# Optimization experiments

Hardware: AMD Instinct MI355X
Metric: run time of the kernel (lower is better)

Reference implementation:

```python
import jax, jax.numpy as jnp
import numpy as np

DIM = 6
HID = 8
N_UT = DIM * (DIM - 1) // 2  # 15


def setup_inputs() -> dict:
    key = jax.random.key(0)
    ks = jax.random.split(key, 13)
    B, T = 256, 4096
    x = jax.random.normal(ks[0], (B, T, DIM), dtype=jnp.float32)

    def kaiming(k, fan_out, fan_in):
        std = np.sqrt(2.0 / fan_in)
        return jax.random.normal(k, (fan_out, fan_in), dtype=jnp.float32) * std

    inp = {
        "x": x,
        "W_in": kaiming(ks[1], HID, DIM),
        "b_in": jnp.zeros((HID,), jnp.float32),
        "W1": kaiming(ks[2], HID, HID), "b1": jnp.zeros((HID,), jnp.float32),
        "W2": kaiming(ks[3], HID, HID), "b2": jnp.zeros((HID,), jnp.float32),
        "W3": kaiming(ks[4], HID, HID), "b3": jnp.zeros((HID,), jnp.float32),
        "W4": kaiming(ks[5], HID, HID), "b4": jnp.zeros((HID,), jnp.float32),
        "W_out": kaiming(ks[6], N_UT, HID),
        "b_out": jnp.zeros((N_UT,), jnp.float32),
    }
    return inp


def reference(x, W_in, b_in, W1, b1, W2, b2, W3, b3, W4, b4, W_out, b_out):
    B, T, dim = x.shape
    xf = x.reshape(B * T, dim)
    sp = jax.nn.softplus
    y = sp(xf @ W_in.T + b_in)
    y = sp(y @ W1.T + b1)
    y = sp(y @ W2.T + b2)
    y = sp(y @ W3.T + b3)
    y = sp(y @ W4.T + b4)
    ut = y @ W_out.T + b_out  # [N, dim*(dim-1)/2]
    iu, ju = jnp.triu_indices(dim, k=1)  # row-major order matches torch loop
    L = jnp.zeros((B * T, dim, dim), dtype=x.dtype)
    L = L.at[:, iu, ju].set(ut)
    L = L.at[:, ju, iu].set(-ut)
    return L.reshape(B, T, dim, dim)
```

## Files before the change

### kernel.cpp

```cpp
#include <hip/hip_runtime.h>

#define DEV_INLINE __device__ __forceinline__

DEV_INLINE float softplus_f(float v) {
    return fmaxf(v, 0.0f) + __logf(1.0f + __expf(-fabsf(v)));
}

__global__ __launch_bounds__(256) void pb_kernel(
    const float* __restrict__ x,
    const float* __restrict__ W_in, const float* __restrict__ b_in,
    const float* __restrict__ W1,   const float* __restrict__ b1,
    const float* __restrict__ W2,   const float* __restrict__ b2,
    const float* __restrict__ W3,   const float* __restrict__ b3,
    const float* __restrict__ W4,   const float* __restrict__ b4,
    const float* __restrict__ W_out,const float* __restrict__ b_out,
    float* __restrict__ out, int n_pairs)
{
    const int tid = blockIdx.x * blockDim.x + threadIdx.x;
    if (tid >= n_pairs) return;

    const float4* xv = (const float4*)x + (size_t)tid * 3;
    float4 a0 = xv[0];
    float4 a1 = xv[1];
    float4 a2 = xv[2];
    float xin[2][6] = {
        { a0.x, a0.y, a0.z, a0.w, a1.x, a1.y },
        { a1.z, a1.w, a2.x, a2.y, a2.z, a2.w }
    };

    float y[2][8];
    #pragma unroll
    for (int r = 0; r < 2; ++r) {
        #pragma unroll
        for (int o = 0; o < 8; ++o) {
            float acc = b_in[o];
            #pragma unroll
            for (int i = 0; i < 6; ++i)
                acc = fmaf(W_in[o * 6 + i], xin[r][i], acc);
            y[r][o] = softplus_f(acc);
        }
    }

    const float* Ws[4] = { W1, W2, W3, W4 };
    const float* bs[4] = { b1, b2, b3, b4 };
    #pragma unroll
    for (int l = 0; l < 4; ++l) {
        const float* __restrict__ W = Ws[l];
        const float* __restrict__ b = bs[l];
        float t[2][8];
        #pragma unroll
        for (int r = 0; r < 2; ++r) {
            #pragma unroll
            for (int o = 0; o < 8; ++o) {
                float acc = b[o];
                #pragma unroll
                for (int i = 0; i < 8; ++i)
                    acc = fmaf(W[o * 8 + i], y[r][i], acc);
                t[r][o] = softplus_f(acc);
            }
        }
        #pragma unroll
        for (int r = 0; r < 2; ++r)
            #pragma unroll
            for (int o = 0; o < 8; ++o)
                y[r][o] = t[r][o];
    }

    float4* ov = (float4*)out + (size_t)tid * 18;
    #pragma unroll
    for (int r = 0; r < 2; ++r) {
        float u[15];
        #pragma unroll
        for (int o = 0; o < 15; ++o) {
            float acc = b_out[o];
            #pragma unroll
            for (int i = 0; i < 8; ++i)
                acc = fmaf(W_out[o * 8 + i], y[r][i], acc);
            u[o] = acc;
        }

        float L[36];
        #pragma unroll
        for (int i = 0; i < 36; ++i) L[i] = 0.0f;
        int k = 0;
        #pragma unroll
        for (int i = 0; i < 6; ++i) {
            #pragma unroll
            for (int j = i + 1; j < 6; ++j) {
                L[i * 6 + j] = u[k];
                L[j * 6 + i] = -u[k];
                ++k;
            }
        }

        #pragma unroll
        for (int q = 0; q < 9; ++q)
            ov[r * 9 + q] = make_float4(L[4 * q + 0], L[4 * q + 1],
                                        L[4 * q + 2], L[4 * q + 3]);
    }
}

extern "C" void kernel_launch(void* const* d_in, const int* in_sizes, int n_in,
                              void* d_out, int out_size, void* d_ws, size_t ws_size,
                              hipStream_t stream) {
    const float* x     = (const float*)d_in[0];
    const float* W_in  = (const float*)d_in[1];
    const float* b_in  = (const float*)d_in[2];
    const float* W1    = (const float*)d_in[3];
    const float* b1    = (const float*)d_in[4];
    const float* W2    = (const float*)d_in[5];
    const float* b2    = (const float*)d_in[6];
    const float* W3    = (const float*)d_in[7];
    const float* b3    = (const float*)d_in[8];
    const float* W4    = (const float*)d_in[9];
    const float* b4    = (const float*)d_in[10];
    const float* W_out = (const float*)d_in[11];
    const float* b_out = (const float*)d_in[12];
    float* out = (float*)d_out;

    const int N = in_sizes[0] / 6;
    const int n_pairs = N / 2;
    const int block = 256;
    const int grid = (n_pairs + block - 1) / block;

    hipLaunchKernelGGL(pb_kernel, dim3(grid), dim3(block), 0, stream,
                       x, W_in, b_in, W1, b1, W2, b2, W3, b3, W4, b4,
                       W_out, b_out, out, n_pairs);
}
```

Measured before the change: 242.0 us.

## Stage output tiles in shared memory for coalesced stores, one row per thread

```diff
diff --git a/kernel.cpp b/kernel.cpp
--- a/kernel.cpp
+++ b/kernel.cpp
@@ -14,31 +14,26 @@
     const float* __restrict__ W3,   const float* __restrict__ b3,
     const float* __restrict__ W4,   const float* __restrict__ b4,
     const float* __restrict__ W_out,const float* __restrict__ b_out,
-    float* __restrict__ out, int n_pairs)
+    float* __restrict__ out, int n_rows)
 {
-    const int tid = blockIdx.x * blockDim.x + threadIdx.x;
-    if (tid >= n_pairs) return;
+    __shared__ float4 sbuf[256 * 9];
 
-    const float4* xv = (const float4*)x + (size_t)tid * 3;
-    float4 a0 = xv[0];
-    float4 a1 = xv[1];
-    float4 a2 = xv[2];
-    float xin[2][6] = {
-        { a0.x, a0.y, a0.z, a0.w, a1.x, a1.y },
-        { a1.z, a1.w, a2.x, a2.y, a2.z, a2.w }
-    };
+    const int tid = threadIdx.x;
+    const int row_raw = blockIdx.x * 256 + tid;
+    const int row = row_raw < n_rows ? row_raw : n_rows - 1;
 
-    float y[2][8];
+    const float2* xv = (const float2*)(x + (size_t)row * 6);
+    float2 p0 = xv[0], p1 = xv[1], p2 = xv[2];
+    const float xin[6] = { p0.x, p0.y, p1.x, p1.y, p2.x, p2.y };
+
+    float y[8];
     #pragma unroll
-    for (int r = 0; r < 2; ++r) {
+    for (int o = 0; o < 8; ++o) {
+        float acc = b_in[o];
         #pragma unroll
-        for (int o = 0; o < 8; ++o) {
-            float acc = b_in[o];
-            #pragma unroll
-            for (int i = 0; i < 6; ++i)
-                acc = fmaf(W_in[o * 6 + i], xin[r][i], acc);
-            y[r][o] = softplus_f(acc);
-        }
+        for (int i = 0; i < 6; ++i)
+            acc = fmaf(W_in[o * 6 + i], xin[i], acc);
+        y[o] = softplus_f(acc);
     }
 
     const float* Ws[4] = { W1, W2, W3, W4 };
@@ -47,41 +42,33 @@
     for (int l = 0; l < 4; ++l) {
         const float* __restrict__ W = Ws[l];
         const float* __restrict__ b = bs[l];
-        float t[2][8];
+        float t[8];
         #pragma unroll
-        for (int r = 0; r < 2; ++r) {
+        for (int o = 0; o < 8; ++o) {
+            float acc = b[o];
             #pragma unroll
-            for (int o = 0; o < 8; ++o) {
-                float acc = b[o];
-                #pragma unroll
-                for (int i = 0; i < 8; ++i)
-                    acc = fmaf(W[o * 8 + i], y[r][i], acc);
-                t[r][o] = softplus_f(acc);
-            }
+            for (int i = 0; i < 8; ++i)
+                acc = fmaf(W[o * 8 + i], y[i], acc);
+            t[o] = softplus_f(acc);
         }
         #pragma unroll
-        for (int r = 0; r < 2; ++r)
-            #pragma unroll
-            for (int o = 0; o < 8; ++o)
-                y[r][o] = t[r][o];
+        for (int o = 0; o < 8; ++o) y[o] = t[o];
     }
 
-    float4* ov = (float4*)out + (size_t)tid * 18;
+    float u[15];
     #pragma unroll
-    for (int r = 0; r < 2; ++r) {
-        float u[15];
+    for (int o = 0; o < 15; ++o) {
+        float acc = b_out[o];
         #pragma unroll
-        for (int o = 0; o < 15; ++o) {
-            float acc = b_out[o];
-            #pragma unroll
-            for (int i = 0; i < 8; ++i)
-                acc = fmaf(W_out[o * 8 + i], y[r][i], acc);
-            u[o] = acc;
-        }
+        for (int i = 0; i < 8; ++i)
+            acc = fmaf(W_out[o * 8 + i], y[i], acc);
+        u[o] = acc;
+    }
 
-        float L[36];
-        #pragma unroll
-        for (int i = 0; i < 36; ++i) L[i] = 0.0f;
+    float L[36];
+    #pragma unroll
+    for (int i = 0; i < 36; ++i) L[i] = 0.0f;
+    {
         int k = 0;
         #pragma unroll
         for (int i = 0; i < 6; ++i) {
@@ -92,11 +79,23 @@
                 ++k;
             }
         }
+    }
 
-        #pragma unroll
-        for (int q = 0; q < 9; ++q)
-            ov[r * 9 + q] = make_float4(L[4 * q + 0], L[4 * q + 1],
-                                        L[4 * q + 2], L[4 * q + 3]);
+    #pragma unroll
+    for (int m = 0; m < 9; ++m)
+        sbuf[tid * 9 + m] = make_float4(L[4 * m + 0], L[4 * m + 1],
+                                        L[4 * m + 2], L[4 * m + 3]);
+
+    __syncthreads();
+
+    float4* dst = (float4*)out + (size_t)blockIdx.x * (256 * 9);
+    const long long total_f4 = (long long)n_rows * 9;
+    #pragma unroll
+    for (int q = 0; q < 9; ++q) {
+        const int idx = q * 256 + tid;
+        const long long gidx = (long long)blockIdx.x * (256 * 9) + idx;
+        if (gidx < total_f4)
+            dst[idx] = sbuf[idx];
     }
 }
 
@@ -118,12 +117,11 @@
     const float* b_out = (const float*)d_in[12];
     float* out = (float*)d_out;
 
-    const int N = in_sizes[0] / 6;
-    const int n_pairs = N / 2;
+    const int n_rows = in_sizes[0] / 6;
     const int block = 256;
-    const int grid = (n_pairs + block - 1) / block;
+    const int grid = (n_rows + block - 1) / block;
 
     hipLaunchKernelGGL(pb_kernel, dim3(grid), dim3(block), 0, stream,
                        x, W_in, b_in, W1, b1, W2, b2, W3, b3, W4, b4,
-                       W_out, b_out, out, n_pairs);
+                       W_out, b_out, out, n_rows);
 }
```

After: 197.2 us. 1.23x faster.
